# Optimization experiments

Measured on AMD Instinct MI355X. Metric: run time of the kernel, lower is better.

## Reference

```python
import jax, jax.numpy as jnp
import numpy as np

P = 7            # cfg.POOLING_SIZE (= group_size)
N_CLASSES = 21   # PASCAL VOC incl. background
SPATIAL_SCALE = 1.0 / 16.0


def _round_half_up(x):
    # matches C round() for non-negative roi coords (jnp.round is banker's)
    return jnp.floor(x + 0.5)


def psroi_pool(feat, rois, out_dim):
    """Position-sensitive RoI average pooling via integral images.
    feat: [B, out_dim*P*P, H, W]; rois: [N, 5] (batch_idx, x1, y1, x2, y2).
    Returns [N, out_dim, P, P]."""
    B, C, H, W = feat.shape
    # summed-area table, zero-padded: S[b,c,h,w] = sum feat[b,c,:h,:w]
    S = jnp.cumsum(jnp.cumsum(feat, axis=2), axis=3)
    S = jnp.pad(S, ((0, 0), (0, 0), (1, 0), (1, 0)))

    b = rois[:, 0].astype(jnp.int32)
    x1 = _round_half_up(rois[:, 1]) * SPATIAL_SCALE
    y1 = _round_half_up(rois[:, 2]) * SPATIAL_SCALE
    x2 = _round_half_up(rois[:, 3] + 1.0) * SPATIAL_SCALE
    y2 = _round_half_up(rois[:, 4] + 1.0) * SPATIAL_SCALE
    roi_w = jnp.maximum(x2 - x1, 0.1)
    roi_h = jnp.maximum(y2 - y1, 0.1)
    bin_w = roi_w / P
    bin_h = roi_h / P

    g = jnp.arange(P, dtype=feat.dtype)
    hs = jnp.clip(jnp.floor(g[None] * bin_h[:, None] + y1[:, None]), 0, H).astype(jnp.int32)        # [N,P]
    he = jnp.clip(jnp.ceil((g[None] + 1.0) * bin_h[:, None] + y1[:, None]), 0, H).astype(jnp.int32)
    ws = jnp.clip(jnp.floor(g[None] * bin_w[:, None] + x1[:, None]), 0, W).astype(jnp.int32)
    we = jnp.clip(jnp.ceil((g[None] + 1.0) * bin_w[:, None] + x1[:, None]), 0, W).astype(jnp.int32)

    # channel for (ctop, gh, gw) is (ctop*P + gh)*P + gw == arange(C) reshaped
    c = jnp.arange(C, dtype=jnp.int32).reshape(1, out_dim, P, P)
    bi = b[:, None, None, None]
    h0 = hs[:, None, :, None]; h1 = he[:, None, :, None]
    w0 = ws[:, None, None, :]; w1 = we[:, None, None, :]
    # box-sum from integral image -> [N, out_dim, P, P]
    ssum = S[bi, c, h1, w1] - S[bi, c, h0, w1] - S[bi, c, h1, w0] + S[bi, c, h0, w0]

    dh = jnp.maximum(he - hs, 0)[:, None, :, None]
    dw = jnp.maximum(we - ws, 0)[:, None, None, :]
    area = (dh * dw).astype(feat.dtype)
    return jnp.where(area > 0, ssum / jnp.maximum(area, 1.0), 0.0)


def setup_inputs() -> dict:
    key = jax.random.key(0)
    k1, k2, k3, k4, k5 = jax.random.split(key, 5)
    B, Cin, H, W = 4, 2048, 64, 64
    base_feat = jax.random.normal(k1, (B, Cin, H, W), jnp.float32)
    w_conv1 = 0.01 * jax.random.normal(k2, (1024, Cin), jnp.float32)
    w_cls = 0.01 * jax.random.normal(k3, (N_CLASSES * P * P, 1024), jnp.float32)
    w_bbox = 0.001 * jax.random.normal(k4, (4 * N_CLASSES * P * P, 1024), jnp.float32)
    # 300 ROIs per image in image coords (image size = 16*H = 1024)
    n_per = 300
    ka, kb = jax.random.split(k5)
    xy1 = jax.random.uniform(ka, (B * n_per, 2), jnp.float32, 0.0, 900.0)
    wh = jax.random.uniform(kb, (B * n_per, 2), jnp.float32, 16.0, 160.0)
    xy2 = jnp.minimum(xy1 + wh, 1023.0)
    bidx = jnp.repeat(jnp.arange(B, dtype=jnp.float32), n_per)[:, None]
    rois = jnp.concatenate([bidx, xy1[:, 0:1], xy1[:, 1:2], xy2[:, 0:1], xy2[:, 1:2]], axis=1)
    return {"base_feat": base_feat, "rois": rois, "w_conv1": w_conv1, "w_cls": w_cls, "w_bbox": w_bbox}


def reference(base_feat, rois, w_conv1, w_cls, w_bbox):
    B = base_feat.shape[0]
    n_per = rois.shape[0] // B
    # 1x1 conv (no bias) + relu
    x = jax.nn.relu(jnp.einsum('oi,bihw->bohw', w_conv1, base_feat))
    # cls branch: 1x1 conv -> PSRoIPool -> PxP avgpool -> softmax
    cls_feat = jnp.einsum('oi,bihw->bohw', w_cls, x)
    pooled_cls = psroi_pool(cls_feat, rois, N_CLASSES)        # [N, 21, P, P]
    cls_score = pooled_cls.mean(axis=(2, 3))                   # [N, 21]
    cls_prob = jax.nn.softmax(cls_score, axis=1)
    # bbox branch: 1x1 conv -> PSRoIPool -> PxP avgpool
    bbox_feat = jnp.einsum('oi,bihw->bohw', w_bbox, x)
    pooled_loc = psroi_pool(bbox_feat, rois, 4 * N_CLASSES)    # [N, 84, P, P]
    bbox_pred = pooled_loc.mean(axis=(2, 3))                    # [N, 84]
    return cls_prob.reshape(B, n_per, -1), bbox_pred.reshape(B, n_per, -1)
```

## Files before the change

### kernel.cpp

```cpp
#include <hip/hip_runtime.h>
#include <cstdint>


typedef __attribute__((ext_vector_type(8))) short short8;
typedef __attribute__((ext_vector_type(4))) short short4v;
typedef __attribute__((ext_vector_type(4))) float f32x4;

#define OFF_FEATT 0ull
#define OFF_W1    67108864ull
#define OFF_U2    0ull
#define OFF_P2    64225280ull
#define OFF_WC    71303168ull
#define OFF_DESC  84148224ull
#define OFF_SCORE 86155264ull
#define OFF_X     86810624ull
#define OFF_U1    153919488ull
#define OFF_P1    282370048ull
#define ONEPASS_BYTES 296419328ull

__device__ __forceinline__ unsigned short f2bf(float f) {
  unsigned u = __float_as_uint(f);
  u += 0x7fffu + ((u >> 16) & 1u);
  return (unsigned short)(u >> 16);
}
__device__ __forceinline__ float bf2f(unsigned short h) {
  return __uint_as_float(((unsigned)h) << 16);
}

__device__ __forceinline__ int swz6(int k6, int key) {
  return ((((k6 >> 3) & 7) ^ key) << 3) | (k6 & 7);
}

__device__ __forceinline__ void gload16(const void* g, void* l) {
  __builtin_amdgcn_global_load_lds((const __attribute__((address_space(1))) void*)g,
                                   (__attribute__((address_space(3))) void*)l, 16, 0, 0);
}

__global__ __launch_bounds__(256) void k_cvt_w1(const float* __restrict__ src,
                                                unsigned short* __restrict__ dst) {
  int t = blockIdx.x * 256 + threadIdx.x;
  long e = (long)t * 4;
  if (e >= 1024 * 2048) return;
  int o = (int)(e >> 11), k = (int)(e & 2047);
  float4 q = *(const float4*)(src + e);
  short4v s = {(short)f2bf(q.x), (short)f2bf(q.y), (short)f2bf(q.z), (short)f2bf(q.w)};
  int kp = (k & ~63) | swz6(k & 63, o & 7);
  *(short4v*)(dst + (size_t)o * 2048 + kp) = s;
}

__global__ __launch_bounds__(256) void k_cvt_wcomb(const float* __restrict__ wcls,
                                                   const float* __restrict__ wbbox,
                                                   unsigned short* __restrict__ dst) {
  int t = blockIdx.x * 256 + threadIdx.x;
  if (t >= 128 * 49 * 256) return;
  size_t e = (size_t)t * 4;
  int c = (int)(e / 50176);
  int rem = (int)(e - (size_t)c * 50176);
  int ij = rem >> 10, k = rem & 1023;
  float4 q = make_float4(0.f, 0.f, 0.f, 0.f);
  if (c < 21)       q = *(const float4*)(wcls + (size_t)(c * 49 + ij) * 1024 + k);
  else if (c < 105) q = *(const float4*)(wbbox + (size_t)((c - 21) * 49 + ij) * 1024 + k);
  short4v s = {(short)f2bf(q.x), (short)f2bf(q.y), (short)f2bf(q.z), (short)f2bf(q.w)};
  int kp = (k & ~63) | swz6(k & 63, c & 7);
  *(short4v*)(dst + ((size_t)(c * 49 + ij) * 1024 + kp)) = s;
}

__global__ __launch_bounds__(256) void k_tpose(const float* __restrict__ src,
                                               unsigned short* __restrict__ dst) {
  __shared__ float tile[64][65];
  int s0 = blockIdx.x * 64, c0 = blockIdx.y * 64, b = blockIdx.z;
  int tx = threadIdx.x & 63, ty = threadIdx.x >> 6;
  const float* sp = src + ((size_t)b * 2048 + c0) * 4096 + s0;
#pragma unroll
  for (int i = 0; i < 16; i++) {
    int cl = ty * 16 + i;
    tile[cl][tx] = sp[(size_t)cl * 4096 + tx];
  }
  __syncthreads();
  unsigned short* dp = dst + ((size_t)b * 4096 + s0) * 2048 + c0;
  int c4 = (threadIdx.x & 15) * 4;
  int sy = threadIdx.x >> 4;
#pragma unroll
  for (int i = 0; i < 4; i++) {
    int sl = i * 16 + sy;
    int key = sl & 7;
    short4v v = {(short)f2bf(tile[c4 + 0][sl]), (short)f2bf(tile[c4 + 1][sl]),
                 (short)f2bf(tile[c4 + 2][sl]), (short)f2bf(tile[c4 + 3][sl])};
    *(short4v*)(dp + (size_t)sl * 2048 + swz6(c4, key)) = v;
  }
}

__global__ __launch_bounds__(256) void k_gemm_conv1(const short* __restrict__ A,
                                                    const short* __restrict__ Bw,
                                                    float* __restrict__ X) {
  int mt = blockIdx.x, nt = blockIdx.y, b = blockIdx.z;
  __shared__ short As[128 * 64];
  __shared__ short Bs[128 * 64];
  int tid = threadIdx.x, lane = tid & 63, wave = tid >> 6;
  int wm = wave >> 1, wn = wave & 1;
  f32x4 acc[4][4];
#pragma unroll
  for (int i = 0; i < 4; i++)
#pragma unroll
    for (int j = 0; j < 4; j++) acc[i][j] = (f32x4){0.f, 0.f, 0.f, 0.f};

  const short* Ab = A + ((size_t)b * 4096 + (size_t)mt * 128) * 2048;
  const short* Bb = Bw + (size_t)nt * 128 * 2048;
  int lr = lane >> 3;
  int lc = (lane & 7) * 8;
  int key = lane & 7;

  for (int k0 = 0; k0 < 2048; k0 += 64) {
#pragma unroll
    for (int i = 0; i < 4; i++) {
      int row = i * 32 + wave * 8 + lr;
      gload16(Ab + (size_t)row * 2048 + k0 + lc, (char*)As + (i * 32 + wave * 8) * 128);
      gload16(Bb + (size_t)row * 2048 + k0 + lc, (char*)Bs + (i * 32 + wave * 8) * 128);
    }
    __syncthreads();
#pragma unroll
    for (int kt = 0; kt < 2; kt++) {
      int ko = (((kt << 2) | (lane >> 4)) ^ key) << 3;
      short8 af[4], bfr[4];
#pragma unroll
      for (int i = 0; i < 4; i++)
        af[i] = *(const short8*)(As + (wm * 64 + i * 16 + (lane & 15)) * 64 + ko);
#pragma unroll
      for (int j = 0; j < 4; j++)
        bfr[j] = *(const short8*)(Bs + (wn * 64 + j * 16 + (lane & 15)) * 64 + ko);
#pragma unroll
      for (int i = 0; i < 4; i++)
#pragma unroll
        for (int j = 0; j < 4; j++)
          acc[i][j] = __builtin_amdgcn_mfma_f32_16x16x32_bf16(af[i], bfr[j], acc[i][j], 0, 0, 0);
    }
    __syncthreads();
  }
  float* Xb = X + ((size_t)b * 4096 + (size_t)mt * 128) * 1024 + nt * 128;
#pragma unroll
  for (int i = 0; i < 4; i++)
#pragma unroll
    for (int j = 0; j < 4; j++) {
      int row = wm * 64 + i * 16 + (lane >> 4) * 4;
      int col = wn * 64 + j * 16 + (lane & 15);
#pragma unroll
      for (int r = 0; r < 4; r++)
        Xb[(size_t)(row + r) * 1024 + col] = fmaxf(acc[i][j][r], 0.f);
    }
}

__global__ __launch_bounds__(256) void k_desc(const float* __restrict__ rois,
                                              int* __restrict__ desc) {
  int t = blockIdx.x * 256 + threadIdx.x;
  if (t >= 1280 * 49) return;
  int roi = t / 49, ij = t - roi * 49;
  int* d = desc + (size_t)t * 8;
  if (roi >= 1200) { d[0] = 0; d[1] = 0; d[2] = 0; d[3] = 0; d[4] = 0; ((float*)d)[5] = 0.f; return; }
  const float* r = rois + (size_t)roi * 5;
  int b = (int)r[0];
  float x1 = __fmul_rn(floorf(__fadd_rn(r[1], 0.5f)), 0.0625f);
  float y1 = __fmul_rn(floorf(__fadd_rn(r[2], 0.5f)), 0.0625f);
  float x2 = __fmul_rn(floorf(__fadd_rn(__fadd_rn(r[3], 1.0f), 0.5f)), 0.0625f);
  float y2 = __fmul_rn(floorf(__fadd_rn(__fadd_rn(r[4], 1.0f), 0.5f)), 0.0625f);
  float bw = __fdiv_rn(fmaxf(__fsub_rn(x2, x1), 0.1f), 7.0f);
  float bh = __fdiv_rn(fmaxf(__fsub_rn(y2, y1), 0.1f), 7.0f);
  int i = ij / 7, j = ij - (ij / 7) * 7;
  float fi = (float)i, fj = (float)j;
  int hs = (int)fminf(fmaxf(floorf(__fadd_rn(__fmul_rn(fi, bh), y1)), 0.f), 64.f);
  int he = (int)fminf(fmaxf(ceilf(__fadd_rn(__fmul_rn(__fadd_rn(fi, 1.f), bh), y1)), 0.f), 64.f);
  int wsx = (int)fminf(fmaxf(floorf(__fadd_rn(__fmul_rn(fj, bw), x1)), 0.f), 64.f);
  int we = (int)fminf(fmaxf(ceilf(__fadd_rn(__fmul_rn(__fadd_rn(fj, 1.f), bw), x1)), 0.f), 64.f);
  int dh = max(he - hs, 0), dw = max(we - wsx, 0);
  float inv = (dh * dw > 0) ? 1.0f / (float)(dh * dw) : 0.f;
  d[0] = b; d[1] = hs; d[2] = he; d[3] = wsx; d[4] = we;
  ((float*)d)[5] = inv;
}

__global__ __launch_bounds__(256) void k_ubuild(const float* __restrict__ X,
                                                const int* __restrict__ desc,
                                                unsigned short* __restrict__ U) {
  int t = blockIdx.x;
  const int* d = desc + (size_t)t * 8;
  int b = d[0], hs = d[1], he = d[2], wsx = d[3], we = d[4];
  float inv = ((const float*)d)[5];
  int key = (t / 49) & 7;
  int k = threadIdx.x * 4;
  float ax = 0.f, ay = 0.f, az = 0.f, aw = 0.f;
  for (int h = hs; h < he; h++) {
    const float* rowp = X + ((size_t)((b * 64 + h) * 64 + wsx)) * 1024 + k;
    for (int w = wsx; w < we; w++) {
      float4 q = *(const float4*)rowp;
      ax += q.x; ay += q.y; az += q.z; aw += q.w;
      rowp += 1024;
    }
  }
  short4v s = {(short)f2bf(ax * inv), (short)f2bf(ay * inv),
               (short)f2bf(az * inv), (short)f2bf(aw * inv)};
  int kp = (k & ~63) | swz6(k & 63, key);
  *(short4v*)(U + (size_t)t * 1024 + kp) = s;
}

__global__ __launch_bounds__(256) void k_poolgemm2(const unsigned short* __restrict__ U,
                                                   const unsigned short* __restrict__ Wc,
                                                   unsigned short* __restrict__ P,
                                                   int nroi) {
  int mt = blockIdx.x;
  int ij = blockIdx.y;
  __shared__ short As[64 * 64];
  __shared__ short Bs[128 * 64];
  int tid = threadIdx.x, lane = tid & 63, wave = tid >> 6;
  f32x4 acc[4][2];
#pragma unroll
  for (int i = 0; i < 4; i++)
#pragma unroll
    for (int j = 0; j < 2; j++) acc[i][j] = (f32x4){0.f, 0.f, 0.f, 0.f};

  const unsigned short* Ab = U + ((size_t)mt * 64 * 49 + ij) * 1024;
  const unsigned short* Bb = Wc + (size_t)ij * 1024;
  int lr = lane >> 3, lc = (lane & 7) * 8;
  int key = lane & 7;

  for (int k0 = 0; k0 < 1024; k0 += 64) {
#pragma unroll
    for (int i = 0; i < 2; i++) {
      int row = i * 32 + wave * 8 + lr;
      gload16(Ab + (size_t)row * (49 * 1024) + k0 + lc, (char*)As + (i * 32 + wave * 8) * 128);
    }
#pragma unroll
    for (int i = 0; i < 4; i++) {
      int row = i * 32 + wave * 8 + lr;
      gload16(Bb + (size_t)row * (49 * 1024) + k0 + lc, (char*)Bs + (i * 32 + wave * 8) * 128);
    }
    __syncthreads();
#pragma unroll
    for (int kt = 0; kt < 2; kt++) {
      int ko = (((kt << 2) | (lane >> 4)) ^ key) << 3;
      short8 af[4], bfr[2];
#pragma unroll
      for (int i = 0; i < 4; i++)
        af[i] = *(const short8*)(As + (i * 16 + (lane & 15)) * 64 + ko);
#pragma unroll
      for (int j = 0; j < 2; j++)
        bfr[j] = *(const short8*)(Bs + (wave * 32 + j * 16 + (lane & 15)) * 64 + ko);
#pragma unroll
      for (int i = 0; i < 4; i++)
#pragma unroll
        for (int j = 0; j < 2; j++)
          acc[i][j] = __builtin_amdgcn_mfma_f32_16x16x32_bf16(af[i], bfr[j], acc[i][j], 0, 0, 0);
    }
    __syncthreads();
  }
  unsigned short* Pb = P + (size_t)ij * nroi * 112;
#pragma unroll
  for (int i = 0; i < 4; i++)
#pragma unroll
    for (int j = 0; j < 2; j++) {
      int cc = wave * 32 + j * 16 + (lane & 15);
      if (cc < 112) {
        int rbase = mt * 64 + i * 16 + (lane >> 4) * 4;
#pragma unroll
        for (int r = 0; r < 4; r++)
          Pb[(size_t)(rbase + r) * 112 + cc] = f2bf(acc[i][j][r]);
      }
    }
}

__global__ __launch_bounds__(256) void k_reduce(const unsigned short* __restrict__ P,
                                                float* __restrict__ score, int nroi) {
  int t = blockIdx.x * 256 + threadIdx.x;
  if (t >= nroi * 112) return;
  int roi = t / 112, c = t - roi * 112;
  float s = 0.f;
#pragma unroll 7
  for (int ij = 0; ij < 49; ij++) s += bf2f(P[(size_t)ij * nroi * 112 + t]);
  score[(size_t)roi * 128 + c] = s;
}

__global__ __launch_bounds__(256) void k_final(const float* __restrict__ score,
                                               float* __restrict__ out) {
  int t = blockIdx.x * 256 + threadIdx.x;
  if (t < 1200) {
    float s[21];
    float mx = -1e30f;
#pragma unroll
    for (int c = 0; c < 21; c++) {
      s[c] = score[(size_t)t * 128 + c] * (1.f / 49.f);
      mx = fmaxf(mx, s[c]);
    }
    float sum = 0.f;
#pragma unroll
    for (int c = 0; c < 21; c++) { s[c] = expf(s[c] - mx); sum += s[c]; }
    float rs = 1.f / sum;
#pragma unroll
    for (int c = 0; c < 21; c++) out[(size_t)t * 21 + c] = s[c] * rs;
  }
  if (t < 100800) {
    int roi = t / 84, c = t - (t / 84) * 84;
    out[25200 + t] = score[(size_t)roi * 128 + 21 + c] * (1.f / 49.f);
  }
}

extern "C" void kernel_launch(void* const* d_in, const int* in_sizes, int n_in,
                              void* d_out, int out_size, void* d_ws, size_t ws_size,
                              hipStream_t stream) {
  const float* base_feat = (const float*)d_in[0];
  const float* rois      = (const float*)d_in[1];
  const float* w_conv1   = (const float*)d_in[2];
  const float* w_cls     = (const float*)d_in[3];
  const float* w_bbox    = (const float*)d_in[4];
  float* out = (float*)d_out;
  char* ws = (char*)d_ws;

  unsigned short* featT = (unsigned short*)(ws + OFF_FEATT);
  unsigned short* w1b   = (unsigned short*)(ws + OFF_W1);
  unsigned short* Wc    = (unsigned short*)(ws + OFF_WC);
  int*            desc  = (int*)(ws + OFF_DESC);
  float*          score = (float*)(ws + OFF_SCORE);
  float*          X     = (float*)(ws + OFF_X);

  k_cvt_w1<<<2048, 256, 0, stream>>>(w_conv1, w1b);
  k_cvt_wcomb<<<6272, 256, 0, stream>>>(w_cls, w_bbox, Wc);
  k_tpose<<<dim3(64, 32, 4), 256, 0, stream>>>(base_feat, featT);
  k_gemm_conv1<<<dim3(32, 8, 4), 256, 0, stream>>>((const short*)featT, (const short*)w1b, X);
  k_desc<<<245, 256, 0, stream>>>(rois, desc);

  if (ws_size >= ONEPASS_BYTES) {
    unsigned short* U = (unsigned short*)(ws + OFF_U1);
    unsigned short* P = (unsigned short*)(ws + OFF_P1);
    k_ubuild<<<1280 * 49, 256, 0, stream>>>(X, desc, U);
    k_poolgemm2<<<dim3(20, 49), 256, 0, stream>>>(U, Wc, P, 1280);
    k_reduce<<<560, 256, 0, stream>>>(P, score, 1280);
  } else {
    unsigned short* U = (unsigned short*)(ws + OFF_U2);
    unsigned short* P = (unsigned short*)(ws + OFF_P2);
    for (int h = 0; h < 2; h++) {
      k_ubuild<<<640 * 49, 256, 0, stream>>>(X, desc + (size_t)h * 640 * 49 * 8, U);
      k_poolgemm2<<<dim3(10, 49), 256, 0, stream>>>(U, Wc, P, 640);
      k_reduce<<<280, 256, 0, stream>>>(P, score + (size_t)h * 640 * 128, 640);
    }
  }
  k_final<<<394, 256, 0, stream>>>(score, out);
}
```

Baseline: 434.9 us.

## Fuse RoI bin averaging into pooled GEMM and store conv1 output as bf16

Removes the separate k_ubuild pass and its U buffer. The pooled GEMM kernel now computes each RoI bin average directly from the conv1 activations while staging its A tile in shared memory. The conv1 output X is written as bf16 instead of fp32, which halves its footprint and the bandwidth of the many overlapping bin-sum reads. The fused gather runs as scalar loops inside the GEMM's k-loop, so it may stall the MFMA pipeline. Storing the activations in bf16 before summation adds rounding error.

```diff
diff --git a/kernel.cpp b/kernel.cpp
--- a/kernel.cpp
+++ b/kernel.cpp
@@ -8,15 +8,11 @@
 
 #define OFF_FEATT 0ull
 #define OFF_W1    67108864ull
-#define OFF_U2    0ull
-#define OFF_P2    64225280ull
-#define OFF_WC    71303168ull
-#define OFF_DESC  84148224ull
-#define OFF_SCORE 86155264ull
-#define OFF_X     86810624ull
-#define OFF_U1    153919488ull
-#define OFF_P1    282370048ull
-#define ONEPASS_BYTES 296419328ull
+#define OFF_X     71303168ull
+#define OFF_WC    104857600ull
+#define OFF_DESC  117702656ull
+#define OFF_SCORE 119709696ull
+#define OFF_P     0ull
 
 __device__ __forceinline__ unsigned short f2bf(float f) {
   unsigned u = __float_as_uint(f);
@@ -92,7 +88,7 @@
 
 __global__ __launch_bounds__(256) void k_gemm_conv1(const short* __restrict__ A,
                                                     const short* __restrict__ Bw,
-                                                    float* __restrict__ X) {
+                                                    unsigned short* __restrict__ X) {
   int mt = blockIdx.x, nt = blockIdx.y, b = blockIdx.z;
   __shared__ short As[128 * 64];
   __shared__ short Bs[128 * 64];
@@ -136,7 +132,7 @@
     }
     __syncthreads();
   }
-  float* Xb = X + ((size_t)b * 4096 + (size_t)mt * 128) * 1024 + nt * 128;
+  unsigned short* Xo = X + ((size_t)b * 4096 + (size_t)mt * 128) * 1024 + nt * 128;
 #pragma unroll
   for (int i = 0; i < 4; i++)
 #pragma unroll
@@ -145,7 +141,7 @@
       int col = wn * 64 + j * 16 + (lane & 15);
 #pragma unroll
       for (int r = 0; r < 4; r++)
-        Xb[(size_t)(row + r) * 1024 + col] = fmaxf(acc[i][j][r], 0.f);
+        Xo[(size_t)(row + r) * 1024 + col] = f2bf(fmaxf(acc[i][j][r], 0.f));
     }
 }
 
@@ -176,31 +172,8 @@
   ((float*)d)[5] = inv;
 }
 
-__global__ __launch_bounds__(256) void k_ubuild(const float* __restrict__ X,
-                                                const int* __restrict__ desc,
-                                                unsigned short* __restrict__ U) {
-  int t = blockIdx.x;
-  const int* d = desc + (size_t)t * 8;
-  int b = d[0], hs = d[1], he = d[2], wsx = d[3], we = d[4];
-  float inv = ((const float*)d)[5];
-  int key = (t / 49) & 7;
-  int k = threadIdx.x * 4;
-  float ax = 0.f, ay = 0.f, az = 0.f, aw = 0.f;
-  for (int h = hs; h < he; h++) {
-    const float* rowp = X + ((size_t)((b * 64 + h) * 64 + wsx)) * 1024 + k;
-    for (int w = wsx; w < we; w++) {
-      float4 q = *(const float4*)rowp;
-      ax += q.x; ay += q.y; az += q.z; aw += q.w;
-      rowp += 1024;
-    }
-  }
-  short4v s = {(short)f2bf(ax * inv), (short)f2bf(ay * inv),
-               (short)f2bf(az * inv), (short)f2bf(aw * inv)};
-  int kp = (k & ~63) | swz6(k & 63, key);
-  *(short4v*)(U + (size_t)t * 1024 + kp) = s;
-}
-
-__global__ __launch_bounds__(256) void k_poolgemm2(const unsigned short* __restrict__ U,
+__global__ __launch_bounds__(256) void k_fusedpool(const unsigned short* __restrict__ Xb,
+                                                   const int* __restrict__ desc,
                                                    const unsigned short* __restrict__ Wc,
                                                    unsigned short* __restrict__ P,
                                                    int nroi) {
@@ -208,28 +181,61 @@
   int ij = blockIdx.y;
   __shared__ short As[64 * 64];
   __shared__ short Bs[128 * 64];
+  __shared__ int dsc[64][4];
   int tid = threadIdx.x, lane = tid & 63, wave = tid >> 6;
+
+  if (tid < 64) {
+    const int* d = desc + ((size_t)(mt * 64 + tid) * 49 + ij) * 8;
+    int b = d[0], hs = d[1], he = d[2], wsx = d[3], we = d[4];
+    dsc[tid][0] = (b * 64 + hs) * 64 + wsx;
+    dsc[tid][1] = max(he - hs, 0);
+    dsc[tid][2] = max(we - wsx, 0);
+    dsc[tid][3] = d[5];
+  }
+  __syncthreads();
+
   f32x4 acc[4][2];
 #pragma unroll
   for (int i = 0; i < 4; i++)
 #pragma unroll
     for (int j = 0; j < 2; j++) acc[i][j] = (f32x4){0.f, 0.f, 0.f, 0.f};
 
-  const unsigned short* Ab = U + ((size_t)mt * 64 * 49 + ij) * 1024;
   const unsigned short* Bb = Wc + (size_t)ij * 1024;
   int lr = lane >> 3, lc = (lane & 7) * 8;
   int key = lane & 7;
+  int r8 = tid >> 3;
+  int k8 = tid & 7;
 
   for (int k0 = 0; k0 < 1024; k0 += 64) {
-#pragma unroll
-    for (int i = 0; i < 2; i++) {
-      int row = i * 32 + wave * 8 + lr;
-      gload16(Ab + (size_t)row * (49 * 1024) + k0 + lc, (char*)As + (i * 32 + wave * 8) * 128);
-    }
 #pragma unroll
     for (int i = 0; i < 4; i++) {
       int row = i * 32 + wave * 8 + lr;
       gload16(Bb + (size_t)row * (49 * 1024) + k0 + lc, (char*)Bs + (i * 32 + wave * 8) * 128);
+    }
+#pragma unroll
+    for (int p = 0; p < 2; p++) {
+      int r = p * 32 + r8;
+      int cs = dsc[r][0], dh = dsc[r][1], dw = dsc[r][2];
+      float inv = __int_as_float(dsc[r][3]);
+      float a0 = 0.f, a1 = 0.f, a2 = 0.f, a3 = 0.f, a4 = 0.f, a5 = 0.f, a6 = 0.f, a7 = 0.f;
+      const unsigned short* xp = Xb + (size_t)cs * 1024 + k0 + k8 * 8;
+      for (int h = 0; h < dh; h++) {
+        const unsigned short* xq = xp;
+        for (int w = 0; w < dw; w++) {
+          short8 v = *(const short8*)xq;
+          a0 += bf2f((unsigned short)v[0]); a1 += bf2f((unsigned short)v[1]);
+          a2 += bf2f((unsigned short)v[2]); a3 += bf2f((unsigned short)v[3]);
+          a4 += bf2f((unsigned short)v[4]); a5 += bf2f((unsigned short)v[5]);
+          a6 += bf2f((unsigned short)v[6]); a7 += bf2f((unsigned short)v[7]);
+          xq += 1024;
+        }
+        xp += 64 * 1024;
+      }
+      short8 o = {(short)f2bf(a0 * inv), (short)f2bf(a1 * inv),
+                  (short)f2bf(a2 * inv), (short)f2bf(a3 * inv),
+                  (short)f2bf(a4 * inv), (short)f2bf(a5 * inv),
+                  (short)f2bf(a6 * inv), (short)f2bf(a7 * inv)};
+      *(short8*)(As + r * 64 + ((k8 ^ (r & 7)) << 3)) = o;
     }
     __syncthreads();
 #pragma unroll
@@ -313,31 +319,18 @@
 
   unsigned short* featT = (unsigned short*)(ws + OFF_FEATT);
   unsigned short* w1b   = (unsigned short*)(ws + OFF_W1);
+  unsigned short* X     = (unsigned short*)(ws + OFF_X);
   unsigned short* Wc    = (unsigned short*)(ws + OFF_WC);
   int*            desc  = (int*)(ws + OFF_DESC);
   float*          score = (float*)(ws + OFF_SCORE);
-  float*          X     = (float*)(ws + OFF_X);
+  unsigned short* P     = (unsigned short*)(ws + OFF_P);
 
   k_cvt_w1<<<2048, 256, 0, stream>>>(w_conv1, w1b);
   k_cvt_wcomb<<<6272, 256, 0, stream>>>(w_cls, w_bbox, Wc);
   k_tpose<<<dim3(64, 32, 4), 256, 0, stream>>>(base_feat, featT);
   k_gemm_conv1<<<dim3(32, 8, 4), 256, 0, stream>>>((const short*)featT, (const short*)w1b, X);
   k_desc<<<245, 256, 0, stream>>>(rois, desc);
-
-  if (ws_size >= ONEPASS_BYTES) {
-    unsigned short* U = (unsigned short*)(ws + OFF_U1);
-    unsigned short* P = (unsigned short*)(ws + OFF_P1);
-    k_ubuild<<<1280 * 49, 256, 0, stream>>>(X, desc, U);
-    k_poolgemm2<<<dim3(20, 49), 256, 0, stream>>>(U, Wc, P, 1280);
-    k_reduce<<<560, 256, 0, stream>>>(P, score, 1280);
-  } else {
-    unsigned short* U = (unsigned short*)(ws + OFF_U2);
-    unsigned short* P = (unsigned short*)(ws + OFF_P2);
-    for (int h = 0; h < 2; h++) {
-      k_ubuild<<<640 * 49, 256, 0, stream>>>(X, desc + (size_t)h * 640 * 49 * 8, U);
-      k_poolgemm2<<<dim3(10, 49), 256, 0, stream>>>(U, Wc, P, 640);
-      k_reduce<<<280, 256, 0, stream>>>(P, score + (size_t)h * 640 * 128, 640);
-    }
-  }
+  k_fusedpool<<<dim3(20, 49), 256, 0, stream>>>(X, desc, Wc, P, 1280);
+  k_reduce<<<560, 256, 0, stream>>>(P, score, 1280);
   k_final<<<394, 256, 0, stream>>>(score, out);
 }
```

Result: no change. 428.0 us (-1.6%).
